# Performance work log

Measured on AMD Instinct MI355X. Metric: run time of the kernel, lower is better.

The kernel has to match this reference:

```python
import jax, jax.numpy as jnp
import numpy as np

B_, T_, IN_, OUT_, N_ = 16, 4096, 512, 512, 512


def setup_inputs() -> dict:
    key = jax.random.key(0)
    ks = jax.random.split(key, 9)
    u = jax.random.normal(ks[0], (B_, T_, IN_), dtype=jnp.float32)
    # LRU init per original module
    rmin, rmax, max_phase = 0.9, 1.0, 6.283
    u1 = jax.random.uniform(ks[1], (N_,), dtype=jnp.float32)
    u2 = jax.random.uniform(ks[2], (N_,), dtype=jnp.float32)
    nu_log = jnp.log(-0.5 * jnp.log(u1 * (rmax + rmin) * (rmax - rmin) + rmin ** 2))
    theta_log = jnp.log(max_phase * u2)
    Lambda_mod = jnp.exp(-jnp.exp(nu_log))
    gamma_log = jnp.log(jnp.sqrt(1.0 - jnp.square(Lambda_mod)))
    B_re = jax.random.normal(ks[3], (N_, IN_), dtype=jnp.float32) / np.sqrt(2 * IN_)
    B_im = jax.random.normal(ks[4], (N_, IN_), dtype=jnp.float32) / np.sqrt(2 * IN_)
    C_re = jax.random.normal(ks[5], (OUT_, N_), dtype=jnp.float32) / np.sqrt(N_)
    C_im = jax.random.normal(ks[6], (OUT_, N_), dtype=jnp.float32) / np.sqrt(N_)
    D = jax.random.normal(ks[7], (OUT_, IN_), dtype=jnp.float32) / np.sqrt(IN_)
    return {"u": u, "nu_log": nu_log, "theta_log": theta_log, "gamma_log": gamma_log,
            "B_re": B_re, "B_im": B_im, "C_re": C_re, "C_im": C_im, "D": D}


def reference(u, nu_log, theta_log, gamma_log, B_re, B_im, C_re, C_im, D):
    # Lambda: diagonal complex transition, |Lambda| = exp(-exp(nu_log)), angle = exp(theta_log)
    mod = jnp.exp(-jnp.exp(nu_log))             # [N]
    theta = jnp.exp(theta_log)
    Lam = jax.lax.complex(mod * jnp.cos(theta), mod * jnp.sin(theta))  # [N] complex64
    gammas = jnp.exp(gamma_log)                  # [N]
    Bc = jax.lax.complex(B_re, B_im) * gammas[:, None]                 # [N, IN]
    Cc = jax.lax.complex(C_re, C_im)                                   # [OUT, N]

    # input projection: Bu[b,t,n] = sum_i Bc[n,i] * u[b,t,i]
    Bu = jnp.einsum('bti,ni->btn', u.astype(Bc.dtype), Bc)             # [B,T,N] complex

    # diagonal linear recurrence x_t = Lam * x_{t-1} + Bu_t, state starts at 0
    a = jnp.broadcast_to(Lam, Bu.shape)

    def combine(e1, e2):
        a1, b1 = e1
        a2, b2 = e2
        return a1 * a2, a2 * b1 + b2

    _, x = jax.lax.associative_scan(combine, (a, Bu), axis=1)          # x: [B,T,N]

    y = 2.0 * jnp.einsum('btn,on->bto', x, Cc).real + jnp.einsum('bti,oi->bto', u, D)
    return y
```

## Files before the change

### kernel.cpp

```cpp
#include <hip/hip_runtime.h>
#include <hip/hip_bf16.h>
#include <cstdint>
#include <cstddef>


using short8 = __attribute__((ext_vector_type(8))) short;
using f32x4 = __attribute__((ext_vector_type(4))) float;

#define BDIM 16
#define TDIM 4096
#define MTOT (BDIM * TDIM)
#define CHUNK 64
#define NCHUNK (TDIM / CHUNK)

__device__ __forceinline__ unsigned short f2bf(float f) {
    unsigned u = __float_as_uint(f);
    u = u + 0x7FFFu + ((u >> 16) & 1u);
    return (unsigned short)(u >> 16);
}
__device__ __forceinline__ float bflo(unsigned w) { return __uint_as_float(w << 16); }
__device__ __forceinline__ float bfhi(unsigned w) { return __uint_as_float(w & 0xFFFF0000u); }

__device__ __forceinline__ size_t perm_off(int row, int kt, int kp, int rowbytes) {
    int kk = kp >> 5, km = kp & 31;
    int half = km >> 4;
    int g = (km & 15) >> 2, j = km & 3;
    int cc = (kk << 2) | g;
    int c = cc ^ (row & 7);
    return (size_t)row * rowbytes + kt * 128 + (c << 4) + half * 8 + j * 2;
}

__device__ __forceinline__ void gload_lds16(const void* g, void* l) {
    __builtin_amdgcn_global_load_lds((const __attribute__((address_space(1))) void*)g,
                                     (__attribute__((address_space(3))) void*)l, 16, 0, 0);
}

__global__ void prep_w1(const float* __restrict__ B_re, const float* __restrict__ B_im,
                        const float* __restrict__ gamma_log, char* __restrict__ W1) {
    int i = blockIdx.x * 256 + threadIdx.x;
    int r = blockIdx.y;
    int n = r >> 1;
    float gmm = expf(gamma_log[n]);
    float v = (r & 1) ? B_im[n * 512 + i] * gmm : B_re[n * 512 + i] * gmm;
    *(unsigned short*)(W1 + perm_off(r, i >> 6, i & 63, 1024)) = f2bf(v);
}

__global__ void prep_w2(const float* __restrict__ C_re, const float* __restrict__ C_im,
                        const float* __restrict__ D, char* __restrict__ W2) {
    int k = blockIdx.x * 256 + threadIdx.x;
    int o = blockIdx.y;
    float v;
    if (k < 1024) {
        int n = k >> 1;
        v = (k & 1) ? -2.0f * C_im[o * 512 + n] : 2.0f * C_re[o * 512 + n];
    } else {
        v = D[o * 512 + (k - 1024)];
    }
    *(unsigned short*)(W2 + perm_off(o, k >> 6, k & 63, 3072)) = f2bf(v);
}

__global__ void convert_u(const float4* __restrict__ u4, char* __restrict__ Apack) {
    size_t idx = (size_t)blockIdx.x * 256 + threadIdx.x;
    float4 v = u4[idx];
    int row = (int)(idx >> 7);
    int c4 = (int)(idx & 127);
    int kg = 1024 + c4 * 4;
    unsigned lo = (unsigned)f2bf(v.x) | ((unsigned)f2bf(v.y) << 16);
    unsigned hi = (unsigned)f2bf(v.z) | ((unsigned)f2bf(v.w) << 16);
    size_t off = perm_off(row, kg >> 6, kg & 63, 3072);
    *reinterpret_cast<uint2*>(Apack + off) = make_uint2(lo, hi);
}

#define ASM_VMCNT4 asm volatile("s_waitcnt vmcnt(4)" ::: "memory")
#define ASM_VMCNT0 asm volatile("s_waitcnt vmcnt(0)" ::: "memory")
#define ASM_LGKM0  asm volatile("s_waitcnt lgkmcnt(0)" ::: "memory")
#define ASM_LGKM2  asm volatile("s_waitcnt lgkmcnt(2)" ::: "memory")
#define ASM_LGKM4  asm volatile("s_waitcnt lgkmcnt(4)" ::: "memory")
#define SCHED0     __builtin_amdgcn_sched_barrier(0)
#define BARRIER    __builtin_amdgcn_s_barrier()
#define PRIO1      __builtin_amdgcn_s_setprio(1)
#define PRIO0      __builtin_amdgcn_s_setprio(0)

template <int OUT_MODE, int NBN, int LDAB, int LDBB>
__global__ __launch_bounds__(512, 2) void gemm_nt(const char* __restrict__ A,
                                                  const char* __restrict__ Bm,
                                                  void* __restrict__ Cout, int ktiles,
                                                  float2* __restrict__ carry,
                                                  const float* __restrict__ nu_log,
                                                  const float* __restrict__ theta_log) {
    __shared__ __align__(16) char lds[131072];
    const int tid = threadIdx.x;
    const int lane = tid & 63, w = tid >> 6;
    const int bid = blockIdx.x;
    const int cpx = gridDim.x >> 3;
    const int swz = (bid & 7) * cpx + (bid >> 3);
    const int bm = swz / NBN, bn = swz % NBN;
    const int wm = (w >> 2) * 128, wn = (w & 3) * 64;
    const int ml = lane & 15, g = lane >> 4;

    const char* AgrL = A + (size_t)(bm * 256 + w * 16 + (lane >> 3)) * LDAB + (lane & 7) * 16;
    const char* BgrL = Bm + (size_t)(bn * 256 + w * 16 + (lane >> 3)) * LDBB + (lane & 7) * 16;

#define STG_A(h, kt_, q) do {                                                         \
        const char* s_ = AgrL + (size_t)((h) * 128) * LDAB + (size_t)(kt_) * 128;     \
        char* d_ = lds + (q) * 65536 + (h) * 16384 + w * 2048;                        \
        gload_lds16(s_, d_);                                                          \
        gload_lds16(s_ + (size_t)8 * LDAB, d_ + 1024);                                \
    } while (0)
#define STG_B(h, kt_, q) do {                                                         \
        const char* s_ = BgrL + (size_t)((h) * 128) * LDBB + (size_t)(kt_) * 128;     \
        char* d_ = lds + (q) * 65536 + 32768 + (h) * 16384 + w * 2048;                \
        gload_lds16(s_, d_);                                                          \
        gload_lds16(s_ + (size_t)8 * LDBB, d_ + 1024);                                \
    } while (0)

#define RD_A1(bank, mt_, Abase) do {                                                  \
        _Pragma("unroll") for (int kk = 0; kk < 2; ++kk) {                            \
            int r_ = wm + (bank) * 64 + (mt_) * 16 + ml;                              \
            int hf_ = r_ >> 7, rl_ = r_ & 127;                                        \
            afr[mt_][kk] = *reinterpret_cast<const short8*>(                          \
                (Abase) + hf_ * 16384 + rl_ * 128 + ((((kk << 2) | g) ^ (rl_ & 7)) << 4)); \
        } } while (0)
#define RD_B1(nh, ntq, Bbase) do {                                                    \
        _Pragma("unroll") for (int kk = 0; kk < 2; ++kk) {                            \
            int c_ = wn + (nh) * 32 + (ntq) * 16 + ml;                                \
            int hf_ = c_ >> 7, cl_ = c_ & 127;                                        \
            bfr[nh][ntq][kk] = *reinterpret_cast<const short8*>(                      \
                (Bbase) + hf_ * 16384 + cl_ * 128 + ((((kk << 2) | g) ^ (cl_ & 7)) << 4)); \
        } } while (0)

#define MFMA8_MT(mh, mtb, nh)                                                         \
    _Pragma("unroll") for (int kk = 0; kk < 2; ++kk)                                  \
    _Pragma("unroll") for (int mi = 0; mi < 2; ++mi)                                  \
    _Pragma("unroll") for (int nt = 0; nt < 2; ++nt)                                  \
        acc[(mh) * 4 + (mtb) + mi][(nh) * 2 + nt] = __builtin_amdgcn_mfma_f32_16x16x32_bf16( \
            afr[(mtb) + mi][kk], bfr[nh][nt][kk], acc[(mh) * 4 + (mtb) + mi][(nh) * 2 + nt], 0, 0, 0)
#define MFMA8_NT(mh, nh, ntq)                                                         \
    _Pragma("unroll") for (int kk = 0; kk < 2; ++kk)                                  \
    _Pragma("unroll") for (int mt = 0; mt < 4; ++mt)                                  \
        acc[(mh) * 4 + mt][(nh) * 2 + (ntq)] = __builtin_amdgcn_mfma_f32_16x16x32_bf16( \
            afr[mt][kk], bfr[nh][ntq][kk], acc[(mh) * 4 + mt][(nh) * 2 + (ntq)], 0, 0, 0)

    f32x4 acc[8][4] = {};
    short8 afr[4][2];
    short8 bfr[2][2][2];

    const char* A0b = lds;
    const char* B0b = lds + 32768;
    const char* A1b = lds + 65536;
    const char* B1b = lds + 98304;

    STG_A(0, 0, 0); STG_A(1, 0, 0); STG_B(0, 0, 0); STG_B(1, 0, 0);
    STG_B(0, 1, 1); STG_B(1, 1, 1);
    ASM_VMCNT4;
    BARRIER;

    const int NT = ktiles >> 1;
    for (int it = 0; it < NT; ++it) {
        const int t1i = 2 * it + 1, t2i = 2 * it + 2, t3i = 2 * it + 3;
        const bool more = (t2i < ktiles);
        RD_B1(0, 0, B0b); RD_B1(0, 1, B0b);
        RD_A1(0, 0, A0b); RD_A1(0, 1, A0b);
        SCHED0;
        RD_A1(0, 2, A0b); RD_A1(0, 3, A0b);
        STG_A(0, t1i, 1);
        BARRIER;
        ASM_LGKM4; SCHED0;
        PRIO1; MFMA8_MT(0, 0, 0); PRIO0;
        ASM_LGKM0; SCHED0;
        PRIO1; MFMA8_MT(0, 2, 0); PRIO0;
        BARRIER;
        RD_B1(1, 0, B0b);
        SCHED0;
        RD_B1(1, 1, B0b);
        STG_A(1, t1i, 1);
        BARRIER;
        ASM_LGKM2; SCHED0;
        PRIO1; MFMA8_NT(0, 1, 0); PRIO0;
        ASM_LGKM0; SCHED0;
        PRIO1; MFMA8_NT(0, 1, 1); PRIO0;
        BARRIER;
        RD_A1(1, 0, A0b); RD_A1(1, 1, A0b);
        SCHED0;
        RD_A1(1, 2, A0b); RD_A1(1, 3, A0b);
        BARRIER;
        ASM_LGKM4; SCHED0;
        PRIO1; MFMA8_MT(1, 0, 0); PRIO0;
        ASM_LGKM0; SCHED0;
        PRIO1; MFMA8_MT(1, 2, 0); PRIO0;
        BARRIER;
        if (more) { STG_B(0, t2i, 0); STG_B(1, t2i, 0); }
        PRIO1; MFMA8_MT(1, 0, 1); MFMA8_MT(1, 2, 1); PRIO0;
        if (more) { ASM_VMCNT4; } else { ASM_VMCNT0; }
        BARRIER;
        RD_B1(0, 0, B1b); RD_B1(0, 1, B1b);
        RD_A1(0, 0, A1b); RD_A1(0, 1, A1b);
        SCHED0;
        RD_A1(0, 2, A1b); RD_A1(0, 3, A1b);
        if (more) STG_A(0, t2i, 0);
        BARRIER;
        ASM_LGKM4; SCHED0;
        PRIO1; MFMA8_MT(0, 0, 0); PRIO0;
        ASM_LGKM0; SCHED0;
        PRIO1; MFMA8_MT(0, 2, 0); PRIO0;
        BARRIER;
        RD_B1(1, 0, B1b);
        SCHED0;
        RD_B1(1, 1, B1b);
        if (more) STG_A(1, t2i, 0);
        BARRIER;
        ASM_LGKM2; SCHED0;
        PRIO1; MFMA8_NT(0, 1, 0); PRIO0;
        ASM_LGKM0; SCHED0;
        PRIO1; MFMA8_NT(0, 1, 1); PRIO0;
        BARRIER;
        RD_A1(1, 0, A1b); RD_A1(1, 1, A1b);
        SCHED0;
        RD_A1(1, 2, A1b); RD_A1(1, 3, A1b);
        BARRIER;
        ASM_LGKM4; SCHED0;
        PRIO1; MFMA8_MT(1, 0, 0); PRIO0;
        ASM_LGKM0; SCHED0;
        PRIO1; MFMA8_MT(1, 2, 0); PRIO0;
        BARRIER;
        if (more) { STG_B(0, t3i, 1); STG_B(1, t3i, 1); }
        PRIO1; MFMA8_MT(1, 0, 1); MFMA8_MT(1, 2, 1); PRIO0;
        if (more) { ASM_VMCNT4; }
        BARRIER;
    }

    if (OUT_MODE == 0) {
        float* O = (float*)Cout;
#pragma unroll
        for (int mt = 0; mt < 8; ++mt)
#pragma unroll
            for (int nt = 0; nt < 4; ++nt)
#pragma unroll
                for (int r_ = 0; r_ < 4; ++r_) {
                    int grow = bm * 256 + wm + mt * 16 + g * 4 + r_;
                    int gcol = bn * 256 + wn + nt * 16 + ml;
                    O[(size_t)grow * 512 + gcol] = acc[mt][nt][r_];
                }
    } else {
        unsigned short* BuOut = (unsigned short*)Cout;
#pragma unroll
        for (int mt = 0; mt < 8; ++mt)
#pragma unroll
            for (int nt = 0; nt < 4; ++nt)
#pragma unroll
                for (int r_ = 0; r_ < 4; ++r_) {
                    int lrow = wm + mt * 16 + g * 4 + r_;
                    int lcol = wn + nt * 16 + ml;
                    unsigned short hv = f2bf(acc[mt][nt][r_]);
                    *(unsigned short*)(lds + lrow * 512 + lcol * 2) = hv;
                    BuOut[(size_t)(bm * 256 + lrow) * 1024 + bn * 256 + lcol] = hv;
                }
        ASM_LGKM0;
        BARRIER;
        SCHED0;
        int n_local = tid & 127, c_local = tid >> 7;
        int nglob = bn * 128 + n_local;
        float mod = expf(-expf(nu_log[nglob]));
        float th = expf(theta_log[nglob]);
        float s, co;
        sincosf(th, &s, &co);
        float Lre = mod * co, Lim = mod * s;
        const char* base = lds + (c_local * 64) * 512 + n_local * 4;
        float xr = 0.f, xi = 0.f;
#pragma unroll 8
        for (int t = 0; t < 64; ++t) {
            unsigned wv = *reinterpret_cast<const unsigned*>(base + t * 512);
            float nr = fmaf(Lre, xr, fmaf(-Lim, xi, bflo(wv)));
            float ni = fmaf(Lre, xi, fmaf(Lim, xr, bfhi(wv)));
            xr = nr; xi = ni;
        }
        int b = (bm * 256) >> 12;
        int cglob = (((bm * 256) & 4095) >> 6) + c_local;
        carry[(size_t)(b * NCHUNK + cglob) * 512 + nglob] = make_float2(xr, xi);
    }
#undef STG_A
#undef STG_B
#undef RD_A1
#undef RD_B1
#undef MFMA8_MT
#undef MFMA8_NT
}

__global__ void scan_prefix(const float2* __restrict__ carry, const float* __restrict__ nu_log,
                            const float* __restrict__ theta_log, float2* __restrict__ prefix) {
    int q = blockIdx.x * 256 + threadIdx.x;
    int n = q & 511, b = q >> 9;
    float e = expf(nu_log[n]);
    float modL = expf(-(float)CHUNK * e);
    float th = expf(theta_log[n]);
    double ang = fmod((double)CHUNK * (double)th, 6.283185307179586);
    float s, co;
    sincosf((float)ang, &s, &co);
    float Lre = modL * co, Lim = modL * s;
    float pr = 0.f, pi = 0.f;
    for (int c = 0; c < NCHUNK; ++c) {
        size_t idx = (size_t)(b * NCHUNK + c) * 512 + n;
        prefix[idx] = make_float2(pr, pi);
        float2 ev = carry[idx];
        float nr = fmaf(Lre, pr, fmaf(-Lim, pi, ev.x));
        float ni = fmaf(Lre, pi, fmaf(Lim, pr, ev.y));
        pr = nr; pi = ni;
    }
}

__global__ void scan_apply(const unsigned* __restrict__ Bu, const float* __restrict__ nu_log,
                           const float* __restrict__ theta_log, const float2* __restrict__ prefix,
                           char* __restrict__ Apack) {
    int q = blockIdx.x * 256 + threadIdx.x;
    int n = q & 511, c = (q >> 9) & 63, b = q >> 15;
    float mod = expf(-expf(nu_log[n]));
    float th = expf(theta_log[n]);
    float s, co;
    sincosf(th, &s, &co);
    float Lre = mod * co, Lim = mod * s;
    const unsigned* p = Bu + ((size_t)(b * TDIM + c * CHUNK)) * 512 + n;
    float2 pv = prefix[(size_t)(b * NCHUNK + c) * 512 + n];
    float xr = pv.x, xi = pv.y;
    int kp = (2 * n) & 63;
    int kk = kp >> 5, km = kp & 31;
    int half = km >> 4, gg = (km & 15) >> 2, j = km & 3;
    int cc = (kk << 2) | gg;
    int partial = (n >> 5) * 128 + half * 8 + j * 2;
    int row0 = b * TDIM + c * CHUNK;
#pragma unroll 8
    for (int t = 0; t < CHUNK; ++t) {
        unsigned wv = p[(size_t)t * 512];
        float nr = fmaf(Lre, xr, fmaf(-Lim, xi, bflo(wv)));
        float ni = fmaf(Lre, xi, fmaf(Lim, xr, bfhi(wv)));
        xr = nr; xi = ni;
        int row = row0 + t;
        size_t off = (size_t)row * 3072 + ((cc ^ (row & 7)) << 4) + partial;
        *reinterpret_cast<unsigned*>(Apack + off) =
            (unsigned)f2bf(xr) | ((unsigned)f2bf(xi) << 16);
    }
}

extern "C" void kernel_launch(void* const* d_in, const int* in_sizes, int n_in,
                              void* d_out, int out_size, void* d_ws, size_t ws_size,
                              hipStream_t stream) {
    const float* u         = (const float*)d_in[0];
    const float* nu_log    = (const float*)d_in[1];
    const float* theta_log = (const float*)d_in[2];
    const float* gamma_log = (const float*)d_in[3];
    const float* B_re      = (const float*)d_in[4];
    const float* B_im      = (const float*)d_in[5];
    const float* C_re      = (const float*)d_in[6];
    const float* C_im      = (const float*)d_in[7];
    const float* D         = (const float*)d_in[8];

    char* ws = (char*)d_ws;
    char* Apack = ws;
    size_t off = (size_t)MTOT * 3072;
    char* W1 = ws + off; off += 1024 * 1024;
    char* W2 = ws + off; off += 512 * 3072;
    float2* carry  = (float2*)(ws + off); off += (size_t)BDIM * NCHUNK * 512 * 8;
    float2* prefix = (float2*)(ws + off); off += (size_t)BDIM * NCHUNK * 512 * 8;

    unsigned short* Bu = (unsigned short*)d_out;

    prep_w1<<<dim3(2, 1024), 256, 0, stream>>>(B_re, B_im, gamma_log, W1);
    prep_w2<<<dim3(6, 512), 256, 0, stream>>>(C_re, C_im, D, W2);
    convert_u<<<32768, 256, 0, stream>>>((const float4*)u, Apack);
    gemm_nt<1, 4, 3072, 1024><<<1024, 512, 0, stream>>>(Apack + 16 * 128, W1,
                                                        (void*)Bu, 8, carry, nu_log, theta_log);
    scan_prefix<<<32, 256, 0, stream>>>(carry, nu_log, theta_log, prefix);
    scan_apply<<<2048, 256, 0, stream>>>((const unsigned*)Bu, nu_log, theta_log, prefix, Apack);
    gemm_nt<0, 2, 3072, 3072><<<512, 512, 0, stream>>>(Apack, W2, d_out, 24,
                                                       nullptr, nullptr, nullptr);
}
```

Before: 301.8 us.

## Replace ping-pong barrier-heavy GEMM schedule with simple double-buffered loop

Replaces the hand-unrolled two-tile ping-pong main loop, which had many intra-iteration barriers and staggered A/B prefetches, with a single loop over k-tiles. Each iteration computes on the current buffer while issuing global-to-LDS loads for the next tile into the other buffer, then waits with vmcnt(0) and one barrier. This cuts barrier count and simplifies the schedule, but every iteration now fully drains outstanding loads, which can expose memory latency that the staggered vmcnt(4) scheme used to hide.

Result: no change. 300.3 us (-0.5%).

```diff
diff --git a/kernel.cpp b/kernel.cpp
--- a/kernel.cpp
+++ b/kernel.cpp
@@ -71,7 +71,6 @@
     *reinterpret_cast<uint2*>(Apack + off) = make_uint2(lo, hi);
 }
 
-#define ASM_VMCNT4 asm volatile("s_waitcnt vmcnt(4)" ::: "memory")
 #define ASM_VMCNT0 asm volatile("s_waitcnt vmcnt(0)" ::: "memory")
 #define ASM_LGKM0  asm volatile("s_waitcnt lgkmcnt(0)" ::: "memory")
 #define ASM_LGKM2  asm volatile("s_waitcnt lgkmcnt(2)" ::: "memory")
@@ -145,87 +144,42 @@
     short8 afr[4][2];
     short8 bfr[2][2][2];
 
-    const char* A0b = lds;
-    const char* B0b = lds + 32768;
-    const char* A1b = lds + 65536;
-    const char* B1b = lds + 98304;
-
     STG_A(0, 0, 0); STG_A(1, 0, 0); STG_B(0, 0, 0); STG_B(1, 0, 0);
-    STG_B(0, 1, 1); STG_B(1, 1, 1);
-    ASM_VMCNT4;
+    ASM_VMCNT0;
     BARRIER;
 
-    const int NT = ktiles >> 1;
-    for (int it = 0; it < NT; ++it) {
-        const int t1i = 2 * it + 1, t2i = 2 * it + 2, t3i = 2 * it + 3;
-        const bool more = (t2i < ktiles);
-        RD_B1(0, 0, B0b); RD_B1(0, 1, B0b);
-        RD_A1(0, 0, A0b); RD_A1(0, 1, A0b);
+#pragma unroll 2
+    for (int kt = 0; kt < ktiles; ++kt) {
+        const int cur = kt & 1, nq = cur ^ 1;
+        const char* Ab = lds + cur * 65536;
+        const char* Bb = Ab + 32768;
+        const bool more = (kt + 1 < ktiles);
+        RD_B1(0, 0, Bb); RD_B1(0, 1, Bb);
+        RD_A1(0, 0, Ab); RD_A1(0, 1, Ab);
         SCHED0;
-        RD_A1(0, 2, A0b); RD_A1(0, 3, A0b);
-        STG_A(0, t1i, 1);
-        BARRIER;
+        RD_A1(0, 2, Ab); RD_A1(0, 3, Ab);
+        if (more) { STG_A(0, kt + 1, nq); STG_A(1, kt + 1, nq); }
         ASM_LGKM4; SCHED0;
         PRIO1; MFMA8_MT(0, 0, 0); PRIO0;
         ASM_LGKM0; SCHED0;
         PRIO1; MFMA8_MT(0, 2, 0); PRIO0;
-        BARRIER;
-        RD_B1(1, 0, B0b);
+        RD_B1(1, 0, Bb);
         SCHED0;
-        RD_B1(1, 1, B0b);
-        STG_A(1, t1i, 1);
-        BARRIER;
+        RD_B1(1, 1, Bb);
+        if (more) { STG_B(0, kt + 1, nq); STG_B(1, kt + 1, nq); }
         ASM_LGKM2; SCHED0;
         PRIO1; MFMA8_NT(0, 1, 0); PRIO0;
         ASM_LGKM0; SCHED0;
         PRIO1; MFMA8_NT(0, 1, 1); PRIO0;
-        BARRIER;
-        RD_A1(1, 0, A0b); RD_A1(1, 1, A0b);
+        RD_A1(1, 0, Ab); RD_A1(1, 1, Ab);
         SCHED0;
-        RD_A1(1, 2, A0b); RD_A1(1, 3, A0b);
-        BARRIER;
+        RD_A1(1, 2, Ab); RD_A1(1, 3, Ab);
         ASM_LGKM4; SCHED0;
         PRIO1; MFMA8_MT(1, 0, 0); PRIO0;
         ASM_LGKM0; SCHED0;
         PRIO1; MFMA8_MT(1, 2, 0); PRIO0;
-        BARRIER;
-        if (more) { STG_B(0, t2i, 0); STG_B(1, t2i, 0); }
         PRIO1; MFMA8_MT(1, 0, 1); MFMA8_MT(1, 2, 1); PRIO0;
-        if (more) { ASM_VMCNT4; } else { ASM_VMCNT0; }
-        BARRIER;
-        RD_B1(0, 0, B1b); RD_B1(0, 1, B1b);
-        RD_A1(0, 0, A1b); RD_A1(0, 1, A1b);
-        SCHED0;
-        RD_A1(0, 2, A1b); RD_A1(0, 3, A1b);
-        if (more) STG_A(0, t2i, 0);
-        BARRIER;
-        ASM_LGKM4; SCHED0;
-        PRIO1; MFMA8_MT(0, 0, 0); PRIO0;
-        ASM_LGKM0; SCHED0;
-        PRIO1; MFMA8_MT(0, 2, 0); PRIO0;
-        BARRIER;
-        RD_B1(1, 0, B1b);
-        SCHED0;
-        RD_B1(1, 1, B1b);
-        if (more) STG_A(1, t2i, 0);
-        BARRIER;
-        ASM_LGKM2; SCHED0;
-        PRIO1; MFMA8_NT(0, 1, 0); PRIO0;
-        ASM_LGKM0; SCHED0;
-        PRIO1; MFMA8_NT(0, 1, 1); PRIO0;
-        BARRIER;
-        RD_A1(1, 0, A1b); RD_A1(1, 1, A1b);
-        SCHED0;
-        RD_A1(1, 2, A1b); RD_A1(1, 3, A1b);
-        BARRIER;
-        ASM_LGKM4; SCHED0;
-        PRIO1; MFMA8_MT(1, 0, 0); PRIO0;
-        ASM_LGKM0; SCHED0;
-        PRIO1; MFMA8_MT(1, 2, 0); PRIO0;
-        BARRIER;
-        if (more) { STG_B(0, t3i, 1); STG_B(1, t3i, 1); }
-        PRIO1; MFMA8_MT(1, 0, 1); MFMA8_MT(1, 2, 1); PRIO0;
-        if (more) { ASM_VMCNT4; }
+        ASM_VMCNT0;
         BARRIER;
     }
 
```
